# Optimization experiments

Hardware: AMD Instinct MI355X
Metric: run time of the kernel (lower is better)

Reference implementation:

```python
import math
import jax, jax.numpy as jnp
import numpy as np

B, D, H, T = 256, 2048, 4096, 11
H_MAX = 0.05  # max Euler step size, matches ODEsolver_Euler default


def setup_inputs() -> dict:
    key = jax.random.key(0)
    k_z, k_w1, k_u, k_w2 = jax.random.split(key, 4)
    s1 = 1.0 / math.sqrt(D)
    s2 = 1.0 / math.sqrt(H)
    return {
        "z0": jax.random.normal(k_z, (B, D), dtype=jnp.float32),
        "t": jnp.linspace(0.0, 1.0, T, dtype=jnp.float32),
        "W1": jax.random.normal(k_w1, (D, H), dtype=jnp.float32) * s1,
        "b1": jnp.zeros((H,), dtype=jnp.float32),
        "u": jax.random.normal(k_u, (H,), dtype=jnp.float32) * 0.1,
        "W2": jax.random.normal(k_w2, (H, D), dtype=jnp.float32) * s2,
        "b2": jnp.zeros((D,), dtype=jnp.float32),
    }


def _euler_solve(z0, t0, t1, f):
    """Euler ODE solver: n_steps = ceil(|t1-t0|/h_max); note the original
    updates t BEFORE evaluating f (z = z + h*f(z, t+h))."""
    n_steps = int(math.ceil(abs(t1 - t0) / H_MAX))
    h = jnp.float32((t1 - t0) / n_steps)

    def step(carry, _):
        t, z = carry
        t = t + h
        z = z + h * f(z, t)
        return (t, z), None

    (_, z_final), _ = jax.lax.scan(step, (jnp.float32(t0), z0), None, length=n_steps)
    return z_final


def reference(z0, t, W1, b1, u, W2, b2):
    # Step counts are inherently data-dependent on the (host-side) time grid.
    t_np = np.asarray(t, dtype=np.float64)

    def f(z, ti):
        # time-conditioned MLP: dz/dt = tanh(z W1 + b1 + ti*u) W2 + b2
        return jnp.tanh(z @ W1 + b1 + ti * u) @ W2 + b2

    z = z0
    for i in range(t_np.shape[0] - 1):  # loop over fixed, small time grid
        z = _euler_solve(z, t_np[i], t_np[i + 1], f)
    # return_whole_sequence=False -> final hidden state only (z[-1])
    return z
```

## Files before the change

### kernel.cpp

```cpp
#include <hip/hip_runtime.h>
#include <hip/hip_bf16.h>
#include <math.h>

#define BDIM 256
#define DDIM 2048
#define HDIM 4096
#define NINTERVAL 10
#define MAXSUB 3
#define NSLOT (NINTERVAL * MAXSUB)

typedef __attribute__((ext_vector_type(8))) __bf16 bf16x8;
typedef __attribute__((ext_vector_type(4))) float f32x4;
typedef unsigned short ushort_t;
typedef unsigned int uint32;

struct Sched { int valid; float h; float t; };

#define WS_W1T 0ull
#define WS_W2T (WS_W1T + (size_t)HDIM*DDIM*2)
#define WS_ZF  (WS_W2T + (size_t)DDIM*HDIM*2)
#define WS_ZB  (WS_ZF  + (size_t)BDIM*DDIM*4)
#define WS_HB  (WS_ZB  + (size_t)BDIM*DDIM*2)
#define WS_SCHED (WS_HB + (size_t)BDIM*HDIM*2)
#define WS_META  (WS_SCHED + 32 * sizeof(Sched))
#define WS_BIAS  (WS_META + 64)

__device__ inline float bf2f(ushort_t u) {
    union { uint32 ui; float f; } v; v.ui = ((uint32)u) << 16; return v.f;
}
__device__ inline ushort_t f2bf(float f) {
    union { __bf16 b; ushort_t u; } v; v.b = (__bf16)f; return v.u;
}
__device__ inline float tanh_fast(float x) {
    float ax = fabsf(x);
    float e = __expf(-2.0f * ax);
    float t = (1.0f - e) / (1.0f + e);
    return x < 0.0f ? -t : t;
}

typedef __attribute__((address_space(1))) const unsigned int guint;
typedef __attribute__((address_space(3))) unsigned int luint;
__device__ __forceinline__ void gload16(const void* g, void* l) {
    __builtin_amdgcn_global_load_lds((guint*)g, (luint*)l, 16, 0, 0);
}

__global__ void setup_sched(const ushort_t* __restrict__ traw, Sched* __restrict__ sched,
                            int* __restrict__ meta) {
    if (threadIdx.x != 0 || blockIdx.x != 0) return;
    int isbf = (traw[10] == (ushort_t)0x3F80) ? 1 : 0;
    meta[0] = isbf;
    const float* tf = (const float*)traw;
    int cnt = 0;
    for (int i = 0; i < NINTERVAL; ++i) {
        float t0 = isbf ? bf2f(traw[i])     : tf[i];
        float t1 = isbf ? bf2f(traw[i + 1]) : tf[i + 1];
        double d = (double)t1 - (double)t0;
        int n = (int)ceil(fabs(d) / 0.05);
        if (n < 1) n = 1;
        if (n > MAXSUB) n = MAXSUB;
        float h = (float)(d / (double)n);
        float tt = t0;
        for (int k = 0; k < n; ++k) {
            tt = tt + h;
            Sched s; s.valid = 1; s.h = h; s.t = tt;
            sched[cnt++] = s;
        }
    }
    meta[1] = cnt;
    for (int k = cnt; k < NSLOT; ++k) { Sched s; s.valid = 0; s.h = 0.f; s.t = 0.f; sched[k] = s; }
}

__global__ void prep_bias(const void* __restrict__ b1, const void* __restrict__ u,
                          const void* __restrict__ b2, float* __restrict__ biasf,
                          const int* __restrict__ meta) {
    int isbf = meta[0];
    int i = blockIdx.x * blockDim.x + threadIdx.x;
    if (i >= 10240) return;
    const void* src; int off;
    if (i < 4096)      { src = b1; off = i; }
    else if (i < 8192) { src = u;  off = i - 4096; }
    else               { src = b2; off = i - 8192; }
    biasf[i] = isbf ? bf2f(((const ushort_t*)src)[off]) : ((const float*)src)[off];
}

__global__ void init_z(const void* __restrict__ z0raw, float4* __restrict__ zf,
                       ushort4* __restrict__ zb, const int* __restrict__ meta) {
    int isbf = meta[0];
    int i = blockIdx.x * blockDim.x + threadIdx.x;
    float4 f;
    if (isbf) {
        ushort4 v = ((const ushort4*)z0raw)[i];
        f.x = bf2f(v.x); f.y = bf2f(v.y); f.z = bf2f(v.z); f.w = bf2f(v.w);
    } else {
        f = ((const float4*)z0raw)[i];
    }
    zf[i] = f;
    ushort4 o;
    o.x = f2bf(f.x); o.y = f2bf(f.y); o.z = f2bf(f.z); o.w = f2bf(f.w);
    zb[i] = o;
}

__global__ void transpose_any(const void* __restrict__ src, ushort_t* __restrict__ dst,
                              int R, int C, const int* __restrict__ meta) {
    __shared__ ushort_t tile[64][65];
    int isbf = meta[0];
    int c0 = blockIdx.x * 64;
    int r0 = blockIdx.y * 64;
    int tid = threadIdx.x;
    int lr = tid >> 4;
    int lc = (tid & 15) << 2;
    for (int rr = 0; rr < 64; rr += 16) {
        size_t off = (size_t)(r0 + lr + rr) * C + c0 + lc;
        ushort_t e0, e1, e2, e3;
        if (isbf) {
            ushort4 v = *(const ushort4*)((const ushort_t*)src + off);
            e0 = v.x; e1 = v.y; e2 = v.z; e3 = v.w;
        } else {
            float4 v = *(const float4*)((const float*)src + off);
            e0 = f2bf(v.x); e1 = f2bf(v.y); e2 = f2bf(v.z); e3 = f2bf(v.w);
        }
        tile[lr + rr][lc + 0] = e0; tile[lr + rr][lc + 1] = e1;
        tile[lr + rr][lc + 2] = e2; tile[lr + rr][lc + 3] = e3;
    }
    __syncthreads();
    for (int rr = 0; rr < 64; rr += 16) {
        int i = lr + rr;
        ushort4 w;
        w.x = tile[lc + 0][i]; w.y = tile[lc + 1][i];
        w.z = tile[lc + 2][i]; w.w = tile[lc + 3][i];
        *(ushort4*)&dst[(size_t)(c0 + i) * R + r0 + lc] = w;
    }
}


#define BUF1U 16384
__global__ void __launch_bounds__(512)
gemm1_k(const __bf16* __restrict__ zb, const __bf16* __restrict__ w1t,
        const float* __restrict__ biasf, __bf16* __restrict__ hb,
        const Sched* __restrict__ sched, int s, const int* __restrict__ meta) {
    if (s >= meta[1]) return;
    extern __shared__ ushort_t ldsw[];
    Sched sc = sched[s];
    int bid = blockIdx.x;
    int q = bid & 7, j = bid >> 3;
    int nt = q * 8 + (j & 7);
    int mt = j >> 3;
    int m0 = mt * 64, n0 = nt * 64;
    int tid = threadIdx.x;
    int wv = tid >> 6, lane = tid & 63;

    if (wv >= 4) {
        int ptid = (wv - 4) * 64 + lane;
        const __bf16* gA[4]; const __bf16* gB[4];
#pragma unroll
        for (int r = 0; r < 4; ++r) {
            int slot = r * 256 + ptid;
            int row = slot >> 4, cc = (slot & 15) ^ (row & 7);
            gA[r] = zb + (size_t)(m0 + row) * DDIM + cc * 8;
            gB[r] = w1t + (size_t)(n0 + row) * DDIM + cc * 8;
        }
        auto stage = [&](int b, int kt) {
            ushort_t* base = ldsw + b * BUF1U;
#pragma unroll
            for (int r = 0; r < 4; ++r) {
                gload16(gA[r] + kt * 128, base + (size_t)(r * 256 + ptid) * 8);
                gload16(gB[r] + kt * 128, base + 8192 + (size_t)(r * 256 + ptid) * 8);
            }
        };
        stage(0, 0);
        stage(1, 1);
        stage(2, 2);
        asm volatile("s_waitcnt vmcnt(16)" ::: "memory");
#pragma unroll 1
        for (int t = 0; t < 16; ++t) {
            __builtin_amdgcn_s_barrier();
            if (t + 3 < 16) {
                stage((t + 3) & 3, t + 3);
                asm volatile("s_waitcnt vmcnt(16)" ::: "memory");
            } else if (t == 13) {
                asm volatile("s_waitcnt vmcnt(8)" ::: "memory");
            } else if (t == 14) {
                asm volatile("s_waitcnt vmcnt(0)" ::: "memory");
            }
        }
        return;
    }

    int r16 = lane & 15, quad = lane >> 4;
    int mh = wv & 1, nh = wv >> 1;
    int arow0 = mh * 32 + r16, arow1 = arow0 + 16;
    int brow0 = nh * 32 + r16, brow1 = brow0 + 16;
    f32x4 acc[2][2];
#pragma unroll
    for (int a = 0; a < 2; ++a)
#pragma unroll
        for (int b = 0; b < 2; ++b) acc[a][b] = 0;

    auto compute = [&](int b) {
        const ushort_t* bufA = ldsw + b * BUF1U;
        const ushort_t* bufB = bufA + 8192;
#pragma unroll
        for (int kk = 0; kk < 4; ++kk) {
            int c = kk * 4 + quad;
            bf16x8 a0 = *(const bf16x8*)(bufA + (size_t)(arow0 * 16 + (c ^ (arow0 & 7))) * 8);
            bf16x8 a1 = *(const bf16x8*)(bufA + (size_t)(arow1 * 16 + (c ^ (arow1 & 7))) * 8);
            bf16x8 b0 = *(const bf16x8*)(bufB + (size_t)(brow0 * 16 + (c ^ (brow0 & 7))) * 8);
            bf16x8 b1 = *(const bf16x8*)(bufB + (size_t)(brow1 * 16 + (c ^ (brow1 & 7))) * 8);
            acc[0][0] = __builtin_amdgcn_mfma_f32_16x16x32_bf16(a0, b0, acc[0][0], 0, 0, 0);
            acc[0][1] = __builtin_amdgcn_mfma_f32_16x16x32_bf16(a0, b1, acc[0][1], 0, 0, 0);
            acc[1][0] = __builtin_amdgcn_mfma_f32_16x16x32_bf16(a1, b0, acc[1][0], 0, 0, 0);
            acc[1][1] = __builtin_amdgcn_mfma_f32_16x16x32_bf16(a1, b1, acc[1][1], 0, 0, 0);
        }
    };

#pragma unroll 1
    for (int t = 0; t < 16; ++t) {
        __builtin_amdgcn_s_barrier();
        compute(t & 3);
    }

    float te = sc.t;
#pragma unroll
    for (int ni = 0; ni < 2; ++ni) {
        int col = n0 + nh * 32 + ni * 16 + r16;
        float addn = biasf[col] + te * biasf[4096 + col];
#pragma unroll
        for (int mi = 0; mi < 2; ++mi) {
            int rowb = m0 + mh * 32 + mi * 16 + quad * 4;
#pragma unroll
            for (int r = 0; r < 4; ++r)
                hb[(size_t)(rowb + r) * HDIM + col] = (__bf16)tanh_fast(acc[mi][ni][r] + addn);
        }
    }
}

#define BUF2U 24576
__global__ void __launch_bounds__(512)
gemm2_k(const __bf16* __restrict__ hb, const __bf16* __restrict__ w2t,
        const float* __restrict__ biasf, float* __restrict__ zf,
        __bf16* __restrict__ zb, const Sched* __restrict__ sched, int s,
        const int* __restrict__ meta) {
    if (s >= meta[1]) return;
    extern __shared__ ushort_t ldsw[];
    Sched sc = sched[s];
    int bid = blockIdx.x;
    int q = bid & 7, j = bid >> 3;
    int nt = q * 4 + (j & 3);
    int mt = j >> 2;
    int m0 = mt * 32, n0 = nt * 64;
    int tid = threadIdx.x;
    int wv = tid >> 6, lane = tid & 63;

    if (wv >= 4) {
        int ptid = (wv - 4) * 64 + lane;
        const __bf16* gA[4]; const __bf16* gB[8];
#pragma unroll
        for (int r = 0; r < 4; ++r) {
            int slot = r * 256 + ptid;
            int row = slot >> 5, cc = (slot & 31) ^ (row & 7);
            gA[r] = hb + (size_t)(m0 + row) * HDIM + cc * 8;
        }
#pragma unroll
        for (int r = 0; r < 8; ++r) {
            int slot = r * 256 + ptid;
            int row = slot >> 5, cc = (slot & 31) ^ (row & 7);
            gB[r] = w2t + (size_t)(n0 + row) * HDIM + cc * 8;
        }
        auto stage = [&](int b, int kt) {
            ushort_t* base = ldsw + b * BUF2U;
#pragma unroll
            for (int r = 0; r < 4; ++r)
                gload16(gA[r] + kt * 256, base + (size_t)(r * 256 + ptid) * 8);
#pragma unroll
            for (int r = 0; r < 8; ++r)
                gload16(gB[r] + kt * 256, base + 8192 + (size_t)(r * 256 + ptid) * 8);
        };
        stage(0, 0);
        stage(1, 1);
        asm volatile("s_waitcnt vmcnt(12)" ::: "memory");
#pragma unroll 1
        for (int t = 0; t < 16; ++t) {
            __builtin_amdgcn_s_barrier();
            if (t + 2 < 16) {
                stage((t + 2) % 3, t + 2);
                asm volatile("s_waitcnt vmcnt(12)" ::: "memory");
            } else if (t == 14) {
                asm volatile("s_waitcnt vmcnt(0)" ::: "memory");
            }
        }
        return;
    }

    int r16 = lane & 15, quad = lane >> 4;
    int mh = wv & 1, nh = wv >> 1;
    int arow = mh * 16 + r16;
    int brow0 = nh * 32 + r16, brow1 = brow0 + 16;
    f32x4 acc0 = 0, acc1 = 0;

    auto compute = [&](int b) {
        const ushort_t* bufA = ldsw + b * BUF2U;
        const ushort_t* bufB = bufA + 8192;
#pragma unroll
        for (int kk = 0; kk < 8; ++kk) {
            int c = kk * 4 + quad;
            bf16x8 a  = *(const bf16x8*)(bufA + (size_t)(arow * 32 + (c ^ (arow & 7))) * 8);
            bf16x8 b0 = *(const bf16x8*)(bufB + (size_t)(brow0 * 32 + (c ^ (brow0 & 7))) * 8);
            bf16x8 b1 = *(const bf16x8*)(bufB + (size_t)(brow1 * 32 + (c ^ (brow1 & 7))) * 8);
            acc0 = __builtin_amdgcn_mfma_f32_16x16x32_bf16(a, b0, acc0, 0, 0, 0);
            acc1 = __builtin_amdgcn_mfma_f32_16x16x32_bf16(a, b1, acc1, 0, 0, 0);
        }
    };

#pragma unroll 1
    for (int t = 0; t < 16; ++t) {
        __builtin_amdgcn_s_barrier();
        compute(t % 3);
    }

    float hstep = sc.h;
#pragma unroll
    for (int ni = 0; ni < 2; ++ni) {
        int col = n0 + nh * 32 + ni * 16 + r16;
        float b2n = biasf[8192 + col];
        const f32x4& a = (ni == 0) ? acc0 : acc1;
#pragma unroll
        for (int r = 0; r < 4; ++r) {
            int row = m0 + mh * 16 + quad * 4 + r;
            size_t idx = (size_t)row * DDIM + col;
            float nz = zf[idx] + hstep * (a[r] + b2n);
            zf[idx] = nz;
            zb[idx] = (__bf16)nz;
        }
    }
}

__global__ void copy_out(const float4* __restrict__ zf, void* __restrict__ out,
                         const int* __restrict__ meta) {
    int isbf = meta[0];
    int i = blockIdx.x * blockDim.x + threadIdx.x;
    float4 f = zf[i];
    if (isbf) {
        ushort4 o;
        o.x = f2bf(f.x); o.y = f2bf(f.y); o.z = f2bf(f.z); o.w = f2bf(f.w);
        ((ushort4*)out)[i] = o;
    } else {
        ((float4*)out)[i] = f;
    }
}

extern "C" void kernel_launch(void* const* d_in, const int* in_sizes, int n_in,
                              void* d_out, int out_size, void* d_ws, size_t ws_size,
                              hipStream_t stream) {
    const void* z0 = d_in[0];
    const ushort_t* t = (const ushort_t*)d_in[1];
    const void* W1 = d_in[2];
    const void* b1 = d_in[3];
    const void* u  = d_in[4];
    const void* W2 = d_in[5];
    const void* b2 = d_in[6];

    char* ws = (char*)d_ws;
    __bf16* w1t = (__bf16*)(ws + WS_W1T);
    __bf16* w2t = (__bf16*)(ws + WS_W2T);
    float* zf   = (float*)(ws + WS_ZF);
    __bf16* zb  = (__bf16*)(ws + WS_ZB);
    __bf16* hb  = (__bf16*)(ws + WS_HB);
    Sched* sched = (Sched*)(ws + WS_SCHED);
    int* meta = (int*)(ws + WS_META);
    float* biasf = (float*)(ws + WS_BIAS);

    setup_sched<<<1, 64, 0, stream>>>(t, sched, meta);
    prep_bias<<<40, 256, 0, stream>>>(b1, u, b2, biasf, meta);
    init_z<<<512, 256, 0, stream>>>(z0, (float4*)zf, (ushort4*)zb, meta);
    transpose_any<<<dim3(HDIM / 64, DDIM / 64), 256, 0, stream>>>(W1, (ushort_t*)w1t, DDIM, HDIM, meta);
    transpose_any<<<dim3(DDIM / 64, HDIM / 64), 256, 0, stream>>>(W2, (ushort_t*)w2t, HDIM, DDIM, meta);

    for (int s = 0; s < NSLOT; ++s) {
        gemm1_k<<<256, 512, 4 * BUF1U * 2, stream>>>(zb, w1t, biasf, hb, sched, s, meta);
        gemm2_k<<<256, 512, 3 * BUF2U * 2, stream>>>(hb, w2t, biasf, zf, zb, sched, s, meta);
    }
    copy_out<<<512, 256, 0, stream>>>((const float4*)zf, d_out, meta);
}
```

Before: 697.0 us.

## Stage GEMM tiles through producer-wave registers instead of direct global-to-LDS loads

Producer waves in both GEMM kernels now load global tiles into registers, with two register sets in flight, then write them to LDS with ordinary stores. This replaces the direct global_load_lds path. gemm1's LDS ring shrinks from four buffers to three, which lowers its shared-memory footprint. The trade-off is extra LDS write instructions and register pressure in the producer waves, plus a tighter interlock between producers and the barrier schedule.

Result: slower. 896.3 us (+28.6%).

```diff
diff --git a/kernel.cpp b/kernel.cpp
--- a/kernel.cpp
+++ b/kernel.cpp
@@ -11,6 +11,7 @@
 
 typedef __attribute__((ext_vector_type(8))) __bf16 bf16x8;
 typedef __attribute__((ext_vector_type(4))) float f32x4;
+typedef __attribute__((ext_vector_type(4))) unsigned int u32x4;
 typedef unsigned short ushort_t;
 typedef unsigned int uint32;
 
@@ -36,12 +37,6 @@
     float e = __expf(-2.0f * ax);
     float t = (1.0f - e) / (1.0f + e);
     return x < 0.0f ? -t : t;
-}
-
-typedef __attribute__((address_space(1))) const unsigned int guint;
-typedef __attribute__((address_space(3))) unsigned int luint;
-__device__ __forceinline__ void gload16(const void* g, void* l) {
-    __builtin_amdgcn_global_load_lds((guint*)g, (luint*)l, 16, 0, 0);
 }
 
 __global__ void setup_sched(const ushort_t* __restrict__ traw, Sched* __restrict__ sched,
@@ -134,6 +129,7 @@
 
 
 #define BUF1U 16384
+struct RegsP1 { u32x4 a[4]; u32x4 b[4]; };
 __global__ void __launch_bounds__(512)
 gemm1_k(const __bf16* __restrict__ zb, const __bf16* __restrict__ w1t,
         const float* __restrict__ biasf, __bf16* __restrict__ hb,
@@ -159,28 +155,48 @@
             gA[r] = zb + (size_t)(m0 + row) * DDIM + cc * 8;
             gB[r] = w1t + (size_t)(n0 + row) * DDIM + cc * 8;
         }
-        auto stage = [&](int b, int kt) {
+        RegsP1 S0, S1;
+        auto loadr = [&](RegsP1& R, int kt) {
+#pragma unroll
+            for (int r = 0; r < 4; ++r) {
+                R.a[r] = *(const u32x4*)(gA[r] + kt * 128);
+                R.b[r] = *(const u32x4*)(gB[r] + kt * 128);
+            }
+        };
+        auto writebuf = [&](int b, const RegsP1& R) {
             ushort_t* base = ldsw + b * BUF1U;
 #pragma unroll
             for (int r = 0; r < 4; ++r) {
-                gload16(gA[r] + kt * 128, base + (size_t)(r * 256 + ptid) * 8);
-                gload16(gB[r] + kt * 128, base + 8192 + (size_t)(r * 256 + ptid) * 8);
+                *(u32x4*)(base + (size_t)(r * 256 + ptid) * 8) = R.a[r];
+                *(u32x4*)(base + 8192 + (size_t)(r * 256 + ptid) * 8) = R.b[r];
             }
         };
-        stage(0, 0);
-        stage(1, 1);
-        stage(2, 2);
-        asm volatile("s_waitcnt vmcnt(16)" ::: "memory");
+        loadr(S0, 0);
+        loadr(S1, 1);
+        asm volatile("s_waitcnt vmcnt(8)" ::: "memory");
+        writebuf(0, S0);
+        asm volatile("s_waitcnt lgkmcnt(0)" ::: "memory");
 #pragma unroll 1
-        for (int t = 0; t < 16; ++t) {
+        for (int t2 = 0; t2 < 16; t2 += 2) {
             __builtin_amdgcn_s_barrier();
-            if (t + 3 < 16) {
-                stage((t + 3) & 3, t + 3);
-                asm volatile("s_waitcnt vmcnt(16)" ::: "memory");
-            } else if (t == 13) {
+            if (t2 + 2 < 16) {
+                loadr(S0, t2 + 2);
                 asm volatile("s_waitcnt vmcnt(8)" ::: "memory");
-            } else if (t == 14) {
+            } else {
                 asm volatile("s_waitcnt vmcnt(0)" ::: "memory");
+            }
+            writebuf((t2 + 1) % 3, S1);
+            asm volatile("s_waitcnt lgkmcnt(0)" ::: "memory");
+            __builtin_amdgcn_s_barrier();
+            if (t2 + 2 < 16) {
+                if (t2 + 3 < 16) {
+                    loadr(S1, t2 + 3);
+                    asm volatile("s_waitcnt vmcnt(8)" ::: "memory");
+                } else {
+                    asm volatile("s_waitcnt vmcnt(0)" ::: "memory");
+                }
+                writebuf((t2 + 2) % 3, S0);
+                asm volatile("s_waitcnt lgkmcnt(0)" ::: "memory");
             }
         }
         return;
@@ -216,7 +232,7 @@
 #pragma unroll 1
     for (int t = 0; t < 16; ++t) {
         __builtin_amdgcn_s_barrier();
-        compute(t & 3);
+        compute(t % 3);
     }
 
     float te = sc.t;
@@ -235,6 +251,7 @@
 }
 
 #define BUF2U 24576
+struct RegsP2 { u32x4 a[4]; u32x4 b[8]; };
 __global__ void __launch_bounds__(512)
 gemm2_k(const __bf16* __restrict__ hb, const __bf16* __restrict__ w2t,
         const float* __restrict__ biasf, float* __restrict__ zf,
@@ -266,26 +283,50 @@
             int row = slot >> 5, cc = (slot & 31) ^ (row & 7);
             gB[r] = w2t + (size_t)(n0 + row) * HDIM + cc * 8;
         }
-        auto stage = [&](int b, int kt) {
+        RegsP2 S0, S1;
+        auto loadr = [&](RegsP2& R, int kt) {
+#pragma unroll
+            for (int r = 0; r < 4; ++r)
+                R.a[r] = *(const u32x4*)(gA[r] + kt * 256);
+#pragma unroll
+            for (int r = 0; r < 8; ++r)
+                R.b[r] = *(const u32x4*)(gB[r] + kt * 256);
+        };
+        auto writebuf = [&](int b, const RegsP2& R) {
             ushort_t* base = ldsw + b * BUF2U;
 #pragma unroll
             for (int r = 0; r < 4; ++r)
-                gload16(gA[r] + kt * 256, base + (size_t)(r * 256 + ptid) * 8);
+                *(u32x4*)(base + (size_t)(r * 256 + ptid) * 8) = R.a[r];
 #pragma unroll
             for (int r = 0; r < 8; ++r)
-                gload16(gB[r] + kt * 256, base + 8192 + (size_t)(r * 256 + ptid) * 8);
+                *(u32x4*)(base + 8192 + (size_t)(r * 256 + ptid) * 8) = R.b[r];
         };
-        stage(0, 0);
-        stage(1, 1);
+        loadr(S0, 0);
+        loadr(S1, 1);
         asm volatile("s_waitcnt vmcnt(12)" ::: "memory");
+        writebuf(0, S0);
+        asm volatile("s_waitcnt lgkmcnt(0)" ::: "memory");
 #pragma unroll 1
-        for (int t = 0; t < 16; ++t) {
+        for (int t2 = 0; t2 < 16; t2 += 2) {
             __builtin_amdgcn_s_barrier();
-            if (t + 2 < 16) {
-                stage((t + 2) % 3, t + 2);
+            if (t2 + 2 < 16) {
+                loadr(S0, t2 + 2);
                 asm volatile("s_waitcnt vmcnt(12)" ::: "memory");
-            } else if (t == 14) {
+            } else {
                 asm volatile("s_waitcnt vmcnt(0)" ::: "memory");
+            }
+            writebuf((t2 + 1) % 3, S1);
+            asm volatile("s_waitcnt lgkmcnt(0)" ::: "memory");
+            __builtin_amdgcn_s_barrier();
+            if (t2 + 2 < 16) {
+                if (t2 + 3 < 16) {
+                    loadr(S1, t2 + 3);
+                    asm volatile("s_waitcnt vmcnt(12)" ::: "memory");
+                } else {
+                    asm volatile("s_waitcnt vmcnt(0)" ::: "memory");
+                }
+                writebuf((t2 + 2) % 3, S0);
+                asm volatile("s_waitcnt lgkmcnt(0)" ::: "memory");
             }
         }
         return;
@@ -376,7 +417,7 @@
     transpose_any<<<dim3(DDIM / 64, HDIM / 64), 256, 0, stream>>>(W2, (ushort_t*)w2t, HDIM, DDIM, meta);
 
     for (int s = 0; s < NSLOT; ++s) {
-        gemm1_k<<<256, 512, 4 * BUF1U * 2, stream>>>(zb, w1t, biasf, hb, sched, s, meta);
+        gemm1_k<<<256, 512, 3 * BUF1U * 2, stream>>>(zb, w1t, biasf, hb, sched, s, meta);
         gemm2_k<<<256, 512, 3 * BUF2U * 2, stream>>>(hb, w2t, biasf, zf, zb, sched, s, meta);
     }
     copy_out<<<512, 256, 0, stream>>>((const float4*)zf, d_out, meta);
```
